# Kernel tuning notes

Measured on AMD Instinct MI355X. Metric: run time of the kernel, lower is better.

Reference implementation:

```python
import jax, jax.numpy as jnp
import numpy as np

BS, T_SCALE, DUR, EXPAND, RES, CH = 4, 200, 64, 0.5, 16, 128
# max adaptive samples per bin: ceil(max_roi_len / resolution), max_roi_len = 2*DUR-1
MAX_N = int(np.ceil((2 * DUR - 1) / RES))  # = 8 (static)


def make_anchors():
    # Faithful replication of AlignLayer._get_anchors (static, data-independent).
    anchors = []
    for k in range(BS):
        for s in range(T_SCALE):
            for di in range(DUR):
                if s + di < T_SCALE:
                    cl = float(di) + 1.0  # center length
                    anchors.append([k, s - cl * EXPAND, s + di + cl * EXPAND])
                else:
                    anchors.append([k, 0.0, 0.0])
    return jnp.asarray(np.array(anchors, dtype=np.float32))  # [R, 3]


def setup_inputs() -> dict:
    key = jax.random.key(0)
    x = jax.random.normal(key, (BS, CH, T_SCALE), dtype=jnp.float32)
    return {"x": x, "anchors": make_anchors()}


def align1d(x, anchors, resolution=RES, max_n=MAX_N):
    """1D RoI-Align (Align1DLayer semantics, sampling_ratio=0 -> adaptive ceil).
    x: [bs, C, T]; anchors: [R, 3] = (batch_idx, start, end).
    Returns [R, resolution, C]."""
    bs, C, T = x.shape
    b = anchors[:, 0].astype(jnp.int32)              # [R]
    s, e = anchors[:, 1], anchors[:, 2]
    roi_len = jnp.maximum(e - s, 1.0)                # [R]
    bin_size = roi_len / resolution                  # [R]
    n = jnp.ceil(roi_len / resolution)               # [R] adaptive samples/bin (>=1)
    i = jnp.arange(resolution, dtype=jnp.float32)    # bin index
    xf = x.transpose(0, 2, 1).reshape(bs * T, C)     # flat [bs*T, C] for gathers
    base = (b * T)[:, None]                          # [R, 1]
    acc = jnp.zeros((anchors.shape[0], resolution, C), dtype=x.dtype)
    for j in range(max_n):  # small static loop (8), masked per-roi
        # sample coordinate for bin i, sample j
        y = s[:, None] + i[None, :] * bin_size[:, None] \
            + (j + 0.5) * bin_size[:, None] / n[:, None]        # [R, res]
        valid = (y >= -1.0) & (y <= T) & (j < n[:, None])       # kernel range test + adaptive count
        yc = jnp.clip(y, 0.0, None)
        y_lo_f = jnp.floor(yc)
        at_end = y_lo_f >= (T - 1)
        y_lo = jnp.clip(y_lo_f.astype(jnp.int32), 0, T - 1)
        y_hi = jnp.clip(y_lo + 1, 0, T - 1)
        ly = jnp.where(at_end, 0.0, yc - y_lo_f)                # interp weight
        v = (1.0 - ly)[..., None] * xf[base + y_lo] \
            + ly[..., None] * xf[base + y_hi]                   # [R, res, C]
        acc = acc + jnp.where(valid[..., None], v, 0.0)
    return acc / n[:, None, None]


def reference(x, anchors):
    bs, ch, t = x.shape
    feats = align1d(x, anchors)                      # [R, res, C]
    feats = feats.transpose(0, 2, 1)                 # [R, C, res] (matches torch layout)
    feat = feats.reshape(bs, t, DUR, ch * RES)       # view(bs, t, d, -1)
    return feat.transpose(0, 3, 2, 1)                # [bs, C*res, d, t]
```

## Files before the change

kernel.cpp:

```cpp
#include <hip/hip_runtime.h>


#define T_SC 200
#define CH   128
#define ROWF 68
#define OUT_CSTRIDE 204800

__global__ __launch_bounds__(512, 4) void align1d_kernel(
    const float* __restrict__ x, float* __restrict__ out) {
  __shared__ float lds[T_SC * ROWF];

  const int tid   = threadIdx.x;
  const int blk   = blockIdx.x;
  const int k     = blk >> 10;
  const int rem   = blk & 1023;
  const int chalf = rem >> 9;
  const int slice = rem & 511;

  const float* xk = x + (size_t)(k * CH + chalf * 64) * T_SC;
  #pragma unroll
  for (int it = 0; it < 25; ++it) {
    int idx = tid + it * 512;
    int cl  = idx / T_SC;
    int t   = idx - cl * T_SC;
    lds[t * ROWF + cl] = xk[cl * T_SC + t];
  }
  __syncthreads();

  const int wid  = tid >> 6;
  const int lane = tid & 63;
  const int gw   = slice * 8 + wid;
  const int di   = (gw * 23) & 63;
  const int q    = gw >> 6;
  const int ib   = q >> 2;
  const int chnk = q & 3;
  const int s    = chnk * 64 + lane;
  if (s >= T_SC) return;

  const bool  av  = (s + di) < T_SC;
  const float sa  = av ? ((float)s - (float)(di + 1) * 0.5f) : 0.0f;
  const float roi = av ? (float)(2 * di + 1) : 1.0f;
  const float bin = roi * 0.0625f;
  const int   n_l = av ? ((di >> 3) + 1) : 1;
  const int   n0  = (di >> 3) + 1;
  const float n_f = (float)n_l;
  const float inv_n  = __fdiv_rn(1.0f, n_f);
  const float base_y = __fadd_rn(sa, __fmul_rn((float)ib, bin));

  int   aoff_lo[8], aoff_hi[8];
  float w_lo[8], w_hi[8];
  #pragma unroll
  for (int j = 0; j < 8; ++j) {
    aoff_lo[j] = 0; aoff_hi[j] = 0; w_lo[j] = 0.0f; w_hi[j] = 0.0f;
    if (j < n0) {
      float y  = __fadd_rn(base_y,
                   __fdiv_rn(__fmul_rn((float)j + 0.5f, bin), n_f));
      bool ok  = (y >= -1.0f) & (y <= 200.0f) & (j < n_l);
      float yc = fmaxf(y, 0.0f);
      float yl = floorf(yc);
      int  lo  = (int)yl; lo = (lo > T_SC - 1) ? (T_SC - 1) : lo;
      float ly = (yl >= (float)(T_SC - 1)) ? 0.0f : (yc - yl);
      int  hi  = lo + 1;  hi = (hi > T_SC - 1) ? (T_SC - 1) : hi;
      w_lo[j] = ok ? (1.0f - ly) : 0.0f;
      w_hi[j] = ok ? ly : 0.0f;
      aoff_lo[j] = lo * (ROWF * 4);
      aoff_hi[j] = hi * (ROWF * 4);
    }
  }

  const char* ldsc = (const char*)lds;
  size_t obase = (((size_t)(k * 2048 + ib) * 64 + di) * 200 + s)
               + (size_t)(chalf * 64) * OUT_CSTRIDE;
  float* op = out + obase;

  for (int cb = 0; cb < 16; ++cb) {
    const int coff = cb * 16;
    float a0 = 0.0f, a1 = 0.0f, a2 = 0.0f, a3 = 0.0f;
    #pragma unroll
    for (int j = 0; j < 8; ++j) {
      if (j < n0) {
        float4 vl = *(const float4*)(ldsc + aoff_lo[j] + coff);
        float4 vh = *(const float4*)(ldsc + aoff_hi[j] + coff);
        a0 += w_lo[j] * vl.x + w_hi[j] * vh.x;
        a1 += w_lo[j] * vl.y + w_hi[j] * vh.y;
        a2 += w_lo[j] * vl.z + w_hi[j] * vh.z;
        a3 += w_lo[j] * vl.w + w_hi[j] * vh.w;
      }
    }
    float* o = op + (size_t)cb * 4 * OUT_CSTRIDE;
    o[0]               = a0 * inv_n;
    o[OUT_CSTRIDE]     = a1 * inv_n;
    o[2 * OUT_CSTRIDE] = a2 * inv_n;
    o[3 * OUT_CSTRIDE] = a3 * inv_n;
  }
}

extern "C" void kernel_launch(void* const* d_in, const int* in_sizes, int n_in,
                              void* d_out, int out_size, void* d_ws, size_t ws_size,
                              hipStream_t stream) {
  const float* x = (const float*)d_in[0];
  float* out = (float*)d_out;
  align1d_kernel<<<4096, 512, 0, stream>>>(x, out);
}
```

Before: 482.1 us.

## Split channels into quarters, remap warps to avoid idle lanes, vectorize LDS fill

Each block now handles 32 channels instead of 64, which halves the LDS tile and raises launch bounds to 8 blocks per CU, and the grid grows to 6400 blocks. The warp-to-(di, ib, s) mapping is rewritten so no lanes exit early: the last 8 timesteps are packed across bins instead of leaving 56 lanes idle. The global-to-LDS fill uses float4 loads, a zero pad row replaces the hi-index clamp so the hi sample is the lo address plus one row, and the 1/n factor is folded into the weights. Correctness now relies on the zero pad row and on the weight being zero when the clamp would have applied, and each block refills LDS for fewer outputs.

```diff
diff --git a/kernel.cpp b/kernel.cpp
--- a/kernel.cpp
+++ b/kernel.cpp
@@ -2,40 +2,51 @@
 
 
 #define T_SC 200
-#define CH   128
-#define ROWF 68
+#define ROWF 36
 #define OUT_CSTRIDE 204800
 
-__global__ __launch_bounds__(512, 4) void align1d_kernel(
+__global__ __launch_bounds__(512, 8) void align1d_kernel(
     const float* __restrict__ x, float* __restrict__ out) {
-  __shared__ float lds[T_SC * ROWF];
+  __shared__ float lds[(T_SC + 1) * ROWF];
 
-  const int tid   = threadIdx.x;
-  const int blk   = blockIdx.x;
-  const int k     = blk >> 10;
-  const int rem   = blk & 1023;
-  const int chalf = rem >> 9;
-  const int slice = rem & 511;
+  const int tid = threadIdx.x;
+  const int b   = blockIdx.x;
+  const int kcg = b / 400;
+  const int r   = b - kcg * 400;
+  const int k   = kcg >> 2;
+  const int cg  = kcg & 3;
 
-  const float* xk = x + (size_t)(k * CH + chalf * 64) * T_SC;
+  const float4* xk4 = (const float4*)(x + (size_t)(k * 128 + cg * 32) * T_SC);
   #pragma unroll
-  for (int it = 0; it < 25; ++it) {
+  for (int it = 0; it < 4; ++it) {
     int idx = tid + it * 512;
-    int cl  = idx / T_SC;
-    int t   = idx - cl * T_SC;
-    lds[t * ROWF + cl] = xk[cl * T_SC + t];
+    if (idx < 1600) {
+      float4 v = xk4[idx];
+      int c  = idx / 50;
+      int t4 = (idx - c * 50) * 4;
+      float* dst = &lds[t4 * ROWF + c];
+      dst[0]        = v.x;
+      dst[ROWF]     = v.y;
+      dst[2 * ROWF] = v.z;
+      dst[3 * ROWF] = v.w;
+    }
   }
+  if (tid < ROWF) lds[T_SC * ROWF + tid] = 0.0f;
   __syncthreads();
 
   const int wid  = tid >> 6;
   const int lane = tid & 63;
-  const int gw   = slice * 8 + wid;
-  const int di   = (gw * 23) & 63;
-  const int q    = gw >> 6;
-  const int ib   = q >> 2;
-  const int chnk = q & 3;
-  const int s    = chnk * 64 + lane;
-  if (s >= T_SC) return;
+  const int gw   = r * 8 + wid;
+  const int di   = gw / 50;
+  const int sub  = gw - di * 50;
+  int ib, s;
+  if (sub < 48) {
+    ib = sub & 15;
+    s  = (sub >> 4) * 64 + lane;
+  } else {
+    ib = (sub - 48) * 8 + (lane >> 3);
+    s  = 192 + (lane & 7);
+  }
 
   const bool  av  = (s + di) < T_SC;
   const float sa  = av ? ((float)s - (float)(di + 1) * 0.5f) : 0.0f;
@@ -47,11 +58,12 @@
   const float inv_n  = __fdiv_rn(1.0f, n_f);
   const float base_y = __fadd_rn(sa, __fmul_rn((float)ib, bin));
 
-  int   aoff_lo[8], aoff_hi[8];
-  float w_lo[8], w_hi[8];
+  const char* ldsc = (const char*)lds;
+  int   aoff[8];
+  float wl[8], wh[8];
   #pragma unroll
   for (int j = 0; j < 8; ++j) {
-    aoff_lo[j] = 0; aoff_hi[j] = 0; w_lo[j] = 0.0f; w_hi[j] = 0.0f;
+    aoff[j] = 0; wl[j] = 0.0f; wh[j] = 0.0f;
     if (j < n0) {
       float y  = __fadd_rn(base_y,
                    __fdiv_rn(__fmul_rn((float)j + 0.5f, bin), n_f));
@@ -60,38 +72,34 @@
       float yl = floorf(yc);
       int  lo  = (int)yl; lo = (lo > T_SC - 1) ? (T_SC - 1) : lo;
       float ly = (yl >= (float)(T_SC - 1)) ? 0.0f : (yc - yl);
-      int  hi  = lo + 1;  hi = (hi > T_SC - 1) ? (T_SC - 1) : hi;
-      w_lo[j] = ok ? (1.0f - ly) : 0.0f;
-      w_hi[j] = ok ? ly : 0.0f;
-      aoff_lo[j] = lo * (ROWF * 4);
-      aoff_hi[j] = hi * (ROWF * 4);
+      wl[j] = ok ? (1.0f - ly) * inv_n : 0.0f;
+      wh[j] = ok ? ly * inv_n : 0.0f;
+      aoff[j] = lo * (ROWF * 4);
     }
   }
 
-  const char* ldsc = (const char*)lds;
-  size_t obase = (((size_t)(k * 2048 + ib) * 64 + di) * 200 + s)
-               + (size_t)(chalf * 64) * OUT_CSTRIDE;
-  float* op = out + obase;
+  size_t obase = (((size_t)(k * 2048 + cg * 512 + ib) * 64 + di) * 200 + s);
 
-  for (int cb = 0; cb < 16; ++cb) {
+  for (int cb = 0; cb < 8; ++cb) {
     const int coff = cb * 16;
     float a0 = 0.0f, a1 = 0.0f, a2 = 0.0f, a3 = 0.0f;
     #pragma unroll
     for (int j = 0; j < 8; ++j) {
       if (j < n0) {
-        float4 vl = *(const float4*)(ldsc + aoff_lo[j] + coff);
-        float4 vh = *(const float4*)(ldsc + aoff_hi[j] + coff);
-        a0 += w_lo[j] * vl.x + w_hi[j] * vh.x;
-        a1 += w_lo[j] * vl.y + w_hi[j] * vh.y;
-        a2 += w_lo[j] * vl.z + w_hi[j] * vh.z;
-        a3 += w_lo[j] * vl.w + w_hi[j] * vh.w;
+        const char* pj = ldsc + (aoff[j] + coff);
+        float4 vl = *(const float4*)pj;
+        float4 vh = *(const float4*)(pj + ROWF * 4);
+        a0 = fmaf(wl[j], vl.x, fmaf(wh[j], vh.x, a0));
+        a1 = fmaf(wl[j], vl.y, fmaf(wh[j], vh.y, a1));
+        a2 = fmaf(wl[j], vl.z, fmaf(wh[j], vh.z, a2));
+        a3 = fmaf(wl[j], vl.w, fmaf(wh[j], vh.w, a3));
       }
     }
-    float* o = op + (size_t)cb * 4 * OUT_CSTRIDE;
-    o[0]               = a0 * inv_n;
-    o[OUT_CSTRIDE]     = a1 * inv_n;
-    o[2 * OUT_CSTRIDE] = a2 * inv_n;
-    o[3 * OUT_CSTRIDE] = a3 * inv_n;
+    float* o = out + obase + (size_t)cb * 4 * OUT_CSTRIDE;
+    o[0]               = a0;
+    o[OUT_CSTRIDE]     = a1;
+    o[2 * OUT_CSTRIDE] = a2;
+    o[3 * OUT_CSTRIDE] = a3;
   }
 }
 
@@ -100,5 +108,5 @@
                               hipStream_t stream) {
   const float* x = (const float*)d_in[0];
   float* out = (float*)d_out;
-  align1d_kernel<<<4096, 512, 0, stream>>>(x, out);
+  align1d_kernel<<<6400, 512, 0, stream>>>(x, out);
 }
```

Result: slower. 987.1 us (+104.8%).
